# Optimization experiments

Hardware: AMD Instinct MI355X
Metric: run time of the kernel (lower is better)

Reference implementation:

```python
import jax, jax.numpy as jnp
import numpy as np

B, D, H, W = 16, 96, 96, 96
NUM_POINTS = 4096
THRESH = 0.5
CH = [3, 64, 128, 256, 512]   # shared-MLP channel progression (3 mlp layers + global_dim)
GROUPS = 8
EPS = 1e-5
HEAD_HIDDEN = 128


def setup_inputs() -> dict:
    key = jax.random.key(0)
    ks = jax.random.split(key, 8)
    inp = {"volume": jax.random.uniform(ks[0], (B, 1, D, H, W), jnp.float32)}
    for i in range(4):
        # Conv1d(kernel=1, no bias) weight (out, in); kaiming normal fan_out -> std=sqrt(2/out)
        inp[f"w{i+1}"] = jax.random.normal(ks[1 + i], (CH[i + 1], CH[i]), jnp.float32) * np.sqrt(2.0 / CH[i + 1]).astype(np.float32)
        inp[f"gn{i+1}_w"] = jnp.ones((CH[i + 1],), jnp.float32)
        inp[f"gn{i+1}_b"] = jnp.zeros((CH[i + 1],), jnp.float32)
    inp["fc1_w"] = jax.random.normal(ks[5], (HEAD_HIDDEN, CH[-1]), jnp.float32) * np.sqrt(2.0 / HEAD_HIDDEN).astype(np.float32)
    inp["fc1_b"] = jnp.zeros((HEAD_HIDDEN,), jnp.float32)
    inp["fc2_w"] = jax.random.normal(ks[6], (1, HEAD_HIDDEN), jnp.float32) * np.sqrt(2.0).astype(np.float32)
    inp["fc2_b"] = jnp.zeros((1,), jnp.float32)
    return inp


def volume_to_points(volume):
    """Batched, jit-safe version of volume_to_pointcloud (eval mode: linspace sampling)."""
    b, _, d, h, w = volume.shape
    mask = (volume[:, 0] > THRESH).reshape(b, -1)              # (B, D*H*W)
    n = mask.sum(axis=1)                                        # (B,) foreground counts
    # Stable argsort on ~mask puts foreground flat-indices first, in ascending order
    # == torch nonzero() ordering (row-major over D,H,W).
    order = jnp.argsort(jnp.logical_not(mask), axis=1, stable=True)  # (B, D*H*W)
    p = jnp.arange(NUM_POINTS)
    n_f = n.astype(jnp.float32)[:, None]
    # torch.linspace(0, n-1, P).long(): truncation toward zero
    lin = (p[None, :].astype(jnp.float32) * (n_f - 1.0) / (NUM_POINTS - 1)).astype(jnp.int32)
    lin = jnp.clip(lin, 0, jnp.maximum(n[:, None] - 1, 0))
    wrap = p[None, :] % jnp.maximum(n[:, None], 1)              # n < P fallback
    idx = jnp.where(n[:, None] >= NUM_POINTS, lin, wrap)        # (B, P)
    flat = jnp.take_along_axis(order, idx, axis=1)              # (B, P) flat voxel indices
    dd = flat // (h * w)
    hh = (flat // w) % h
    ww = flat % w
    coords = jnp.stack([dd, hh, ww], axis=1).astype(jnp.float32)  # (B, 3, P)
    scale = jnp.array([max(d - 1, 1), max(h - 1, 1), max(w - 1, 1)], jnp.float32)
    pts = coords / scale[None, :, None] * 2.0 - 1.0
    return jnp.where((n > 0)[:, None, None], pts, 0.0)


def group_norm(x, gamma, beta):
    b, c, npts = x.shape
    xg = x.reshape(b, GROUPS, c // GROUPS, npts)
    mu = xg.mean(axis=(2, 3), keepdims=True)
    var = xg.var(axis=(2, 3), keepdims=True)
    xn = ((xg - mu) * jax.lax.rsqrt(var + EPS)).reshape(b, c, npts)
    return xn * gamma[None, :, None] + beta[None, :, None]


def reference(volume, w1, gn1_w, gn1_b, w2, gn2_w, gn2_b, w3, gn3_w, gn3_b,
              w4, gn4_w, gn4_b, fc1_w, fc1_b, fc2_w, fc2_b):
    x = volume_to_points(volume)                                 # (B, 3, P)
    for cw, gw, gb in ((w1, gn1_w, gn1_b), (w2, gn2_w, gn2_b),
                       (w3, gn3_w, gn3_b), (w4, gn4_w, gn4_b)):
        x = jax.nn.relu(group_norm(jnp.einsum('oc,bcn->bon', cw, x), gw, gb))
    g = x.max(axis=2)                                            # (B, 512) global max-pool
    hdn = jax.nn.relu(g @ fc1_w.T + fc1_b)                       # dropout is identity in eval
    logits = (hdn @ fc2_w.T + fc2_b)[:, 0]                       # squeeze(-1) -> (B,)
    return logits
```

## Files before the change

### kernel.cpp

```cpp
#include <hip/hip_runtime.h>
#include <hip/hip_bf16.h>

#define NB 16
#define VOX 884736
#define NPTS 4096
#define CHUNK 1024
#define NCHUNK 864

typedef _Float16 f16x8 __attribute__((ext_vector_type(8)));
typedef _Float16 f16x4 __attribute__((ext_vector_type(4)));
typedef float f32x4 __attribute__((ext_vector_type(4)));

typedef const __attribute__((address_space(1))) _Float16 gf16;
typedef __attribute__((address_space(3))) _Float16 lf16;
#define GLOAD_LDS(gp, lp) __builtin_amdgcn_global_load_lds((gf16*)(gp), (lf16*)(lp), 16, 0, 0)

__device__ __forceinline__ f16x8 nrelu(f16x8 y, f16x8 sc, f16x8 sh) {
    f16x8 r = y * sc + sh;
    #pragma unroll
    for (int e = 0; e < 8; e++) r[e] = (r[e] > (_Float16)0.f) ? r[e] : (_Float16)0.f;
    return r;
}


__device__ inline void cast_chunk(const float* __restrict__ wf, _Float16* __restrict__ wh,
                                  int CIN, int t) {
    int lane = t & 63;
    int NCB = CIN / 32;
    int cb = (t >> 6) % NCB;
    int ob = t / (64 * NCB);
    int o = ob * 16 + (lane & 15);
    int c0 = cb * 32 + (lane >> 4) * 8;
    const float* src = wf + (size_t)o * CIN + c0;
    f16x8 v;
    #pragma unroll
    for (int e = 0; e < 8; e++) v[e] = (_Float16)src[e];
    *(f16x8*)(wh + (size_t)t * 8) = v;
}


__global__ __launch_bounds__(256) void count_cast_kernel(const float* __restrict__ vol,
                                                         int* __restrict__ counts,
                                                         unsigned long long* __restrict__ bits,
                                                         const float* __restrict__ w2,
                                                         const float* __restrict__ w3,
                                                         const float* __restrict__ w4,
                                                         _Float16* __restrict__ w2f,
                                                         _Float16* __restrict__ w3f,
                                                         _Float16* __restrict__ w4f) {
    if (blockIdx.x >= NB * NCHUNK) {
        int t = (blockIdx.x - NB * NCHUNK) * 256 + threadIdx.x;
        if (t < 1024) cast_chunk(w2, w2f, 64, t);
        else if (t < 1024 + 4096) cast_chunk(w3, w3f, 128, t - 1024);
        else if (t < 1024 + 4096 + 16384) cast_chunk(w4, w4f, 256, t - 5120);
        return;
    }
    int blk = blockIdx.x;
    const float4* v4 = (const float4*)(vol + (size_t)blk * CHUNK);
    float4 v = v4[threadIdx.x];
    int nib = (v.x > 0.5f) | ((v.y > 0.5f) << 1) | ((v.z > 0.5f) << 2) | ((v.w > 0.5f) << 3);
    __shared__ unsigned char nibs[256];
    nibs[threadIdx.x] = (unsigned char)nib;
    int cnt = __popc(nib);
    for (int off = 32; off; off >>= 1) cnt += __shfl_down(cnt, off, 64);
    __shared__ int s[4];
    if ((threadIdx.x & 63) == 0) s[threadIdx.x >> 6] = cnt;
    __syncthreads();
    if (threadIdx.x < 16) {
        unsigned long long wd = 0;
        #pragma unroll
        for (int i = 0; i < 16; i++)
            wd |= (unsigned long long)nibs[threadIdx.x * 16 + i] << (4 * i);
        bits[(size_t)blk * 16 + threadIdx.x] = wd;
    }
    if (threadIdx.x == 0) counts[blk] = s[0] + s[1] + s[2] + s[3];
}


__global__ __launch_bounds__(256) void points_kernel(const unsigned long long* __restrict__ bits,
                                                     const int* __restrict__ counts,
                                                     const float* __restrict__ w1,
                                                     float* __restrict__ pts,
                                                     float* __restrict__ pstat1) {
    int b = blockIdx.x >> 4;
    int pc = blockIdx.x & 15;
    int p = pc * 256 + threadIdx.x;
    int tid = threadIdx.x;
    __shared__ int sdat[NCHUNK];
    __shared__ float sw1[192];
    __shared__ int wsum[4];
    for (int i = tid; i < NCHUNK; i += 256) sdat[i] = counts[b * NCHUNK + i];
    if (tid < 192) sw1[tid] = w1[tid];
    __syncthreads();
    int i0 = tid * 4;
    int v0 = (i0 + 0 < NCHUNK) ? sdat[i0 + 0] : 0;
    int v1 = (i0 + 1 < NCHUNK) ? sdat[i0 + 1] : 0;
    int v2 = (i0 + 2 < NCHUNK) ? sdat[i0 + 2] : 0;
    int v3 = (i0 + 3 < NCHUNK) ? sdat[i0 + 3] : 0;
    int l3 = v0 + v1 + v2 + v3;
    int lane = tid & 63, wv = tid >> 6;
    int a = l3;
    #pragma unroll
    for (int off = 1; off < 64; off <<= 1) {
        int x = __shfl_up(a, off, 64);
        if (lane >= off) a += x;
    }
    if (lane == 63) wsum[wv] = a;
    __syncthreads();
    int woff = 0;
    #pragma unroll
    for (int w = 0; w < 4; w++) if (w < wv) woff += wsum[w];
    a += woff;
    int excl = a - l3;
    int n = wsum[0] + wsum[1] + wsum[2] + wsum[3];
    __syncthreads();
    if (i0 + 0 < NCHUNK) sdat[i0 + 0] = excl;
    if (i0 + 1 < NCHUNK) sdat[i0 + 1] = excl + v0;
    if (i0 + 2 < NCHUNK) sdat[i0 + 2] = excl + v0 + v1;
    if (i0 + 3 < NCHUNK) sdat[i0 + 3] = excl + v0 + v1 + v2;
    __syncthreads();
    float px = 0.f, py = 0.f, pz = 0.f;
    if (n > 0) {
        int k;
        if (n >= NPTS) {
            float t = (float)p * ((float)n - 1.0f);
            t = t / 4095.0f;
            k = (int)t;
            if (k > n - 1) k = n - 1;
            if (k < 0) k = 0;
        } else {
            k = p % n;
        }
        int lo = 0, hi = NCHUNK - 1;
        while (lo < hi) {
            int mid = (lo + hi + 1) >> 1;
            if (sdat[mid] <= k) lo = mid; else hi = mid - 1;
        }
        int rr = k - sdat[lo];
        const unsigned long long* wb = bits + ((size_t)b * NCHUNK + lo) * 16;
        unsigned long long chosen = 0;
        int wordidx = 0;
        bool found = false;
        #pragma unroll
        for (int w = 0; w < 16; w++) {
            unsigned long long m = wb[w];
            int pcnt = __popcll(m);
            bool take = (!found) && (rr < pcnt);
            if (take) { chosen = m; wordidx = w; found = true; }
            if (!found) rr -= pcnt;
        }
        int pos = 0;
        unsigned long long m64 = chosen;
        int c = __popcll(m64 & 0xFFFFFFFFull);
        if (rr >= c) { pos = 32; rr -= c; m64 >>= 32; }
        unsigned mm = (unsigned)m64;
        c = __popc(mm & 0xFFFFu); if (rr >= c) { pos += 16; rr -= c; mm >>= 16; }
        c = __popc(mm & 0xFFu);   if (rr >= c) { pos += 8;  rr -= c; mm >>= 8; }
        c = __popc(mm & 0xFu);    if (rr >= c) { pos += 4;  rr -= c; mm >>= 4; }
        c = __popc(mm & 0x3u);    if (rr >= c) { pos += 2;  rr -= c; mm >>= 2; }
        c = mm & 1u;              if (rr >= c) { pos += 1; }
        int flat = lo * CHUNK + wordidx * 64 + pos;
        int dd = flat / 9216;
        int rem = flat - dd * 9216;
        int hh = rem / 96;
        int ww = rem - hh * 96;
        px = (float)dd / 95.0f * 2.0f - 1.0f;
        py = (float)hh / 95.0f * 2.0f - 1.0f;
        pz = (float)ww / 95.0f * 2.0f - 1.0f;
    }
    pts[((size_t)b * 3 + 0) * NPTS + p] = px;
    pts[((size_t)b * 3 + 1) * NPTS + p] = py;
    pts[((size_t)b * 3 + 2) * NPTS + p] = pz;
    float s[8] = {}, q[8] = {};
    #pragma unroll
    for (int o = 0; o < 64; o++) {
        float av = sw1[o * 3 + 0] * px + sw1[o * 3 + 1] * py + sw1[o * 3 + 2] * pz;
        s[o >> 3] += av;
        q[o >> 3] += av * av;
    }
    __shared__ float red[4][8][2];
    #pragma unroll
    for (int g = 0; g < 8; g++) {
        float S = s[g], Q = q[g];
        for (int off = 32; off; off >>= 1) {
            S += __shfl_down(S, off, 64);
            Q += __shfl_down(Q, off, 64);
        }
        if ((threadIdx.x & 63) == 0) { red[wv][g][0] = S; red[wv][g][1] = Q; }
    }
    __syncthreads();
    if (tid < 8) {
        int g = tid;
        float S = red[0][g][0] + red[1][g][0] + red[2][g][0] + red[3][g][0];
        float Q = red[0][g][1] + red[1][g][1] + red[2][g][1] + red[3][g][1];
        float* d = pstat1 + (((size_t)(b * 8 + g)) * 16 + pc) * 2;
        d[0] = S; d[1] = Q;
    }
}


__global__ __launch_bounds__(256, 4) void fused_l2(const float* __restrict__ pts,
                                                   const float* __restrict__ w1,
                                                   const float* __restrict__ pstat1,
                                                   const float* __restrict__ gn1w,
                                                   const float* __restrict__ gn1b,
                                                   const _Float16* __restrict__ wfrag,
                                                   _Float16* __restrict__ y2,
                                                   float* __restrict__ pstat) {
    __shared__ _Float16 sl[64 * 64];
    __shared__ float sw1[192], ssc[64], ssh[64], ms1[8][2];
    int b = blockIdx.y, pblk = blockIdx.x, tid = threadIdx.x;
    if (tid < 192) sw1[tid] = w1[tid];
    if (tid < 8) {
        const float* pbase = pstat1 + (size_t)(b * 8 + tid) * 32;
        float S = 0.f, Q = 0.f;
        #pragma unroll
        for (int pc = 0; pc < 16; pc++) { S += pbase[2 * pc]; Q += pbase[2 * pc + 1]; }
        float inv = 1.0f / (8.0f * 4096.0f);
        float mu = S * inv;
        float var = Q * inv - mu * mu;
        if (var < 0.f) var = 0.f;
        ms1[tid][0] = mu; ms1[tid][1] = rsqrtf(var + 1e-5f);
    }
    __syncthreads();
    if (tid < 64) {
        int g = tid >> 3;
        float ga = gn1w[tid] * ms1[g][1];
        ssc[tid] = ga;
        ssh[tid] = gn1b[tid] - ms1[g][0] * ga;
    }
    __syncthreads();
    {
        int p = tid >> 2, qo = (tid & 3) * 16;
        int pg = pblk * 64 + p;
        float x0 = pts[((size_t)b * 3 + 0) * NPTS + pg];
        float x1 = pts[((size_t)b * 3 + 1) * NPTS + pg];
        float x2 = pts[((size_t)b * 3 + 2) * NPTS + pg];
        #pragma unroll
        for (int e = 0; e < 16; e++) {
            int o = qo + e;
            float a = sw1[o * 3 + 0] * x0 + sw1[o * 3 + 1] * x1 + sw1[o * 3 + 2] * x2;
            float r = fmaxf(a * ssc[o] + ssh[o], 0.f);
            sl[p * 64 + (((o >> 3) ^ (p & 7)) << 3) + (o & 7)] = (_Float16)r;
        }
    }
    __syncthreads();
    int wv = tid >> 6, lane = tid & 63, lr = lane & 15, lk = lane >> 4;
    int ph = wv & 1, oh = wv >> 1;
    int Pg = b * 64 + pblk;
    int pb32 = (Pg << 1) | ph;
    int P16 = Pg * 4 + ph * 2;
    f32x4 acc[2][4] = {};
    #pragma unroll
    for (int cb = 0; cb < 2; cb++) {
        int ch = cb * 4 + lk;
        f16x8 af0, af1;
        {
            int p0 = ph * 32 + lr;
            af0 = *(const f16x8*)(sl + p0 * 64 + ((ch ^ (p0 & 7)) << 3));
            int p1 = p0 + 16;
            af1 = *(const f16x8*)(sl + p1 * 64 + ((ch ^ (p1 & 7)) << 3));
        }
        #pragma unroll
        for (int i = 0; i < 4; i++) {
            int ofr = oh * 4 + i;
            f16x8 bf = *(const f16x8*)(wfrag + (((size_t)ofr * 2 + cb) * 64 + lane) * 8);
            acc[0][i] = __builtin_amdgcn_mfma_f32_16x16x32_f16(bf, af0, acc[0][i], 0, 0, 0);
            acc[1][i] = __builtin_amdgcn_mfma_f32_16x16x32_f16(bf, af1, acc[1][i], 0, 0, 0);
        }
    }
    #pragma unroll
    for (int i = 0; i < 4; i++) {
        int ofr = oh * 4 + i;
        int cb2 = ofr >> 1;
        int kg = (ofr & 1) * 2 + (lk >> 1);
        int lanep = lr + 16 * kg;
        int sub = lk & 1;
        #pragma unroll
        for (int pf = 0; pf < 2; pf++) {
            f16x4 vv;
            #pragma unroll
            for (int j = 0; j < 4; j++) vv[j] = (_Float16)acc[pf][i][j];
            *(f16x4*)(y2 + (((size_t)(P16 + pf) * 4 + cb2) * 64 + lanep) * 8 + sub * 4) = vv;
        }
        float s[4], q[4];
        #pragma unroll
        for (int j = 0; j < 4; j++) {
            float a0 = acc[0][i][j], a1 = acc[1][i][j];
            s[j] = a0 + a1; q[j] = a0 * a0 + a1 * a1;
        }
        #pragma unroll
        for (int m = 1; m <= 8; m <<= 1)
            #pragma unroll
            for (int j = 0; j < 4; j++) {
                s[j] += __shfl_xor(s[j], m, 64);
                q[j] += __shfl_xor(q[j], m, 64);
            }
        if (lr == 0) {
            int o0 = ofr * 16 + lk * 4;
            float* d = pstat + ((size_t)pb32 * 128 + o0) * 2;
            *(float4*)d = make_float4(s[0], q[0], s[1], q[1]);
            *(float4*)(d + 4) = make_float4(s[2], q[2], s[3], q[3]);
        }
    }
}


__global__ __launch_bounds__(256, 4) void fused_l3(const _Float16* __restrict__ y2,
                                                   const float* __restrict__ pstatIn,
                                                   const float* __restrict__ gn2w,
                                                   const float* __restrict__ gn2b,
                                                   const _Float16* __restrict__ w3f,
                                                   _Float16* __restrict__ y3,
                                                   float* __restrict__ pstatOut) {
    __shared__ _Float16 sl[64 * 128];
    __shared__ float sstat[256];
    __shared__ float ms[8][2];
    __shared__ _Float16 sscf[128], sshf[128];
    int b = blockIdx.y, pblk = blockIdx.x, tid = threadIdx.x;
    int wv = tid >> 6, lane = tid & 63, lr = lane & 15, lk = lane >> 4;
    int Pg = b * 64 + pblk;
    const _Float16* yt = y2 + (size_t)Pg * 64 * 128;
    #pragma unroll
    for (int i = 0; i < 4; i++) {
        int off = (wv * 4 + i) * 512;
        GLOAD_LDS(yt + off + lane * 8, sl + off);
    }
    {
        const float* slab = pstatIn + (size_t)b * 128 * 256;
        float acc = 0.f;
        #pragma unroll 8
        for (int pb = 0; pb < 128; pb++) acc += slab[pb * 256 + tid];
        sstat[tid] = acc;
    }
    __syncthreads();
    if (tid < 8) {
        float S = 0.f, Q = 0.f;
        #pragma unroll
        for (int i = 0; i < 16; i++) {
            int c = tid * 16 + i;
            S += sstat[2 * c]; Q += sstat[2 * c + 1];
        }
        float inv = 1.0f / (16.0f * 4096.0f);
        float mu = S * inv;
        float var = Q * inv - mu * mu;
        if (var < 0.f) var = 0.f;
        ms[tid][0] = mu; ms[tid][1] = rsqrtf(var + 1e-5f);
    }
    __syncthreads();
    if (tid < 128) {
        int g = tid >> 4;
        float ga = gn2w[tid] * ms[g][1];
        sscf[tid] = (_Float16)ga;
        sshf[tid] = (_Float16)(gn2b[tid] - ms[g][0] * ga);
    }
    __syncthreads();
    f16x8 scv[4], shv[4];
    #pragma unroll
    for (int cb = 0; cb < 4; cb++) {
        scv[cb] = *(const f16x8*)(sscf + cb * 32 + lk * 8);
        shv[cb] = *(const f16x8*)(sshf + cb * 32 + lk * 8);
    }
    int ph = wv & 1, oh = wv >> 1;
    int pb32 = (Pg << 1) | ph;
    int P16 = Pg * 4 + ph * 2;
    #pragma unroll
    for (int ck = 0; ck < 2; ck++) {
        f32x4 acc[2][4] = {};
        #pragma unroll
        for (int cb = 0; cb < 4; cb++) {
            f16x8 af0 = nrelu(*(const f16x8*)(sl + (((ph * 2 + 0) * 4 + cb) * 64 + lane) * 8), scv[cb], shv[cb]);
            f16x8 af1 = nrelu(*(const f16x8*)(sl + (((ph * 2 + 1) * 4 + cb) * 64 + lane) * 8), scv[cb], shv[cb]);
            #pragma unroll
            for (int i = 0; i < 4; i++) {
                int ofr = oh * 8 + ck * 4 + i;
                f16x8 bf = *(const f16x8*)(w3f + (((size_t)ofr * 4 + cb) * 64 + lane) * 8);
                acc[0][i] = __builtin_amdgcn_mfma_f32_16x16x32_f16(bf, af0, acc[0][i], 0, 0, 0);
                acc[1][i] = __builtin_amdgcn_mfma_f32_16x16x32_f16(bf, af1, acc[1][i], 0, 0, 0);
            }
        }
        #pragma unroll
        for (int i = 0; i < 4; i++) {
            int ofr = oh * 8 + ck * 4 + i;
            int cb3 = ofr >> 1;
            int kg = (ofr & 1) * 2 + (lk >> 1);
            int lanep = lr + 16 * kg;
            int sub = lk & 1;
            #pragma unroll
            for (int pf = 0; pf < 2; pf++) {
                f16x4 vv;
                #pragma unroll
                for (int j = 0; j < 4; j++) vv[j] = (_Float16)acc[pf][i][j];
                *(f16x4*)(y3 + (((size_t)(P16 + pf) * 8 + cb3) * 64 + lanep) * 8 + sub * 4) = vv;
            }
            float s[4], q[4];
            #pragma unroll
            for (int j = 0; j < 4; j++) {
                float a0 = acc[0][i][j], a1 = acc[1][i][j];
                s[j] = a0 + a1; q[j] = a0 * a0 + a1 * a1;
            }
            #pragma unroll
            for (int m = 1; m <= 8; m <<= 1)
                #pragma unroll
                for (int j = 0; j < 4; j++) {
                    s[j] += __shfl_xor(s[j], m, 64);
                    q[j] += __shfl_xor(q[j], m, 64);
                }
            if (lr == 0) {
                int o0 = ofr * 16 + lk * 4;
                float* d = pstatOut + ((size_t)pb32 * 256 + o0) * 2;
                *(float4*)d = make_float4(s[0], q[0], s[1], q[1]);
                *(float4*)(d + 4) = make_float4(s[2], q[2], s[3], q[3]);
            }
        }
    }
}


__global__ __launch_bounds__(256, 4) void fused_l4(const _Float16* __restrict__ y3,
                                                   const float* __restrict__ pstatIn,
                                                   const float* __restrict__ gn3w,
                                                   const float* __restrict__ gn3b,
                                                   const _Float16* __restrict__ w4f,
                                                   float* __restrict__ pstat4) {
    __shared__ _Float16 sl[64 * 256];
    __shared__ float sstat[512];
    __shared__ float ms[8][2];
    __shared__ _Float16 sscf[256], sshf[256];
    int b = blockIdx.y, pblk = blockIdx.x, tid = threadIdx.x;
    int wv = tid >> 6, lane = tid & 63, lr = lane & 15, lk = lane >> 4;
    int Pg = b * 64 + pblk;
    const _Float16* yt = y3 + (size_t)Pg * 64 * 256;
    #pragma unroll
    for (int i = 0; i < 8; i++) {
        int off = (wv * 8 + i) * 512;
        GLOAD_LDS(yt + off + lane * 8, sl + off);
    }
    {
        const float* slab = pstatIn + (size_t)b * 128 * 512;
        float a0 = 0.f, a1 = 0.f;
        #pragma unroll 8
        for (int pb = 0; pb < 128; pb++) {
            a0 += slab[pb * 512 + tid];
            a1 += slab[pb * 512 + tid + 256];
        }
        sstat[tid] = a0;
        sstat[tid + 256] = a1;
    }
    __syncthreads();
    if (tid < 8) {
        float S = 0.f, Q = 0.f;
        #pragma unroll
        for (int i = 0; i < 32; i++) {
            int c = tid * 32 + i;
            S += sstat[2 * c]; Q += sstat[2 * c + 1];
        }
        float inv = 1.0f / (32.0f * 4096.0f);
        float mu = S * inv;
        float var = Q * inv - mu * mu;
        if (var < 0.f) var = 0.f;
        ms[tid][0] = mu; ms[tid][1] = rsqrtf(var + 1e-5f);
    }
    __syncthreads();
    {
        int g = tid >> 5;
        float ga = gn3w[tid] * ms[g][1];
        sscf[tid] = (_Float16)ga;
        sshf[tid] = (_Float16)(gn3b[tid] - ms[g][0] * ga);
    }
    __syncthreads();
    int ph = wv & 1, oh = wv >> 1;
    int pb32 = (Pg << 1) | ph;
    #pragma unroll
    for (int ck = 0; ck < 4; ck++) {
        f32x4 acc[2][4] = {};
        #pragma unroll
        for (int cb = 0; cb < 8; cb++) {
            f16x8 scv = *(const f16x8*)(sscf + cb * 32 + lk * 8);
            f16x8 shv = *(const f16x8*)(sshf + cb * 32 + lk * 8);
            f16x8 af0 = nrelu(*(const f16x8*)(sl + (((ph * 2 + 0) * 8 + cb) * 64 + lane) * 8), scv, shv);
            f16x8 af1 = nrelu(*(const f16x8*)(sl + (((ph * 2 + 1) * 8 + cb) * 64 + lane) * 8), scv, shv);
            #pragma unroll
            for (int i = 0; i < 4; i++) {
                int ofr = oh * 16 + ck * 4 + i;
                f16x8 bf = *(const f16x8*)(w4f + (((size_t)ofr * 8 + cb) * 64 + lane) * 8);
                acc[0][i] = __builtin_amdgcn_mfma_f32_16x16x32_f16(af0, bf, acc[0][i], 0, 0, 0);
                acc[1][i] = __builtin_amdgcn_mfma_f32_16x16x32_f16(af1, bf, acc[1][i], 0, 0, 0);
            }
        }
        #pragma unroll
        for (int i = 0; i < 4; i++) {
            int ofr = oh * 16 + ck * 4 + i;
            float S = 0.f, Q = 0.f, MX = -1e30f, MN = 1e30f;
            #pragma unroll
            for (int pf = 0; pf < 2; pf++)
                #pragma unroll
                for (int j = 0; j < 4; j++) {
                    float v = acc[pf][i][j];
                    S += v; Q += v * v;
                    MX = fmaxf(MX, v); MN = fminf(MN, v);
                }
            S += __shfl_xor(S, 16, 64); Q += __shfl_xor(Q, 16, 64);
            MX = fmaxf(MX, __shfl_xor(MX, 16, 64)); MN = fminf(MN, __shfl_xor(MN, 16, 64));
            S += __shfl_xor(S, 32, 64); Q += __shfl_xor(Q, 32, 64);
            MX = fmaxf(MX, __shfl_xor(MX, 32, 64)); MN = fminf(MN, __shfl_xor(MN, 32, 64));
            if (lk == 0) {
                int o = ofr * 16 + lr;
                *(float4*)(pstat4 + ((size_t)pb32 * 512 + o) * 4) = make_float4(S, Q, MX, MN);
            }
        }
    }
}


__global__ __launch_bounds__(256) void pool_final(const float* __restrict__ pstat4,
                                                  const float* __restrict__ gamma,
                                                  const float* __restrict__ beta,
                                                  float* __restrict__ g) {
    int b = blockIdx.x >> 3, gr = blockIdx.x & 7;
    int ch = threadIdx.x & 63;
    int pg = threadIdx.x >> 6;
    int o = gr * 64 + ch;
    float S = 0.f, Q = 0.f, MX = -1e30f, MN = 1e30f;
    for (int pb = pg; pb < 128; pb += 4) {
        float4 v = *(const float4*)(pstat4 + (((size_t)(b * 128 + pb)) * 512 + o) * 4);
        S += v.x; Q += v.y; MX = fmaxf(MX, v.z); MN = fminf(MN, v.w);
    }
    __shared__ float sS[4][64], sQ[4][64], sMX[4][64], sMN[4][64];
    sS[pg][ch] = S; sQ[pg][ch] = Q; sMX[pg][ch] = MX; sMN[pg][ch] = MN;
    __syncthreads();
    if (threadIdx.x < 64) {
        float Sc = sS[0][ch] + sS[1][ch] + sS[2][ch] + sS[3][ch];
        float Qc = sQ[0][ch] + sQ[1][ch] + sQ[2][ch] + sQ[3][ch];
        float MXc = fmaxf(fmaxf(sMX[0][ch], sMX[1][ch]), fmaxf(sMX[2][ch], sMX[3][ch]));
        float MNc = fminf(fminf(sMN[0][ch], sMN[1][ch]), fminf(sMN[2][ch], sMN[3][ch]));
        float St = Sc, Qt = Qc;
        for (int off = 32; off; off >>= 1) {
            St += __shfl_xor(St, off, 64);
            Qt += __shfl_xor(Qt, off, 64);
        }
        float inv = 1.0f / (64.0f * 4096.0f);
        float mu = St * inv;
        float var = Qt * inv - mu * mu;
        if (var < 0.f) var = 0.f;
        float rstd = rsqrtf(var + 1e-5f);
        float sc = gamma[o] * rstd;
        float sh = beta[o] - mu * sc;
        float m = (sc >= 0.f ? MXc : MNc) * sc + sh;
        g[b * 512 + o] = fmaxf(m, 0.f);
    }
}


__global__ __launch_bounds__(128) void head_kernel(const float* __restrict__ g,
                                                   const float* __restrict__ fc1w,
                                                   const float* __restrict__ fc1b,
                                                   const float* __restrict__ fc2w,
                                                   const float* __restrict__ fc2b,
                                                   float* __restrict__ out) {
    int b = blockIdx.x;
    int o = threadIdx.x;
    __shared__ float sg[512];
    for (int i = threadIdx.x; i < 512; i += 128) sg[i] = g[b * 512 + i];
    __syncthreads();
    float acc = fc1b[o];
    for (int c = 0; c < 512; c++) acc += sg[c] * fc1w[o * 512 + c];
    float h = fmaxf(acc, 0.f) * fc2w[o];
    for (int off = 32; off; off >>= 1) h += __shfl_down(h, off, 64);
    __shared__ float s2[2];
    if ((threadIdx.x & 63) == 0) s2[threadIdx.x >> 6] = h;
    __syncthreads();
    if (threadIdx.x == 0) out[b] = s2[0] + s2[1] + fc2b[0];
}


extern "C" void kernel_launch(void* const* d_in, const int* in_sizes, int n_in,
                              void* d_out, int out_size, void* d_ws, size_t ws_size,
                              hipStream_t stream) {
    const float* vol  = (const float*)d_in[0];
    const float* w1   = (const float*)d_in[1];
    const float* gn1w = (const float*)d_in[2];
    const float* gn1b = (const float*)d_in[3];
    const float* w2   = (const float*)d_in[4];
    const float* gn2w = (const float*)d_in[5];
    const float* gn2b = (const float*)d_in[6];
    const float* w3   = (const float*)d_in[7];
    const float* gn3w = (const float*)d_in[8];
    const float* gn3b = (const float*)d_in[9];
    const float* w4   = (const float*)d_in[10];
    const float* gn4w = (const float*)d_in[11];
    const float* gn4b = (const float*)d_in[12];
    const float* fc1w = (const float*)d_in[13];
    const float* fc1b = (const float*)d_in[14];
    const float* fc2w = (const float*)d_in[15];
    const float* fc2b = (const float*)d_in[16];
    float* out = (float*)d_out;

    char* ws = (char*)d_ws;
    size_t cur = 0;
    auto alloc = [&](size_t bytes) -> void* {
        cur = (cur + 255) & ~(size_t)255;
        void* p = ws + cur;
        cur += bytes;
        return p;
    };
    int*      counts  = (int*)alloc((size_t)NB * NCHUNK * 4);
    unsigned long long* bits = (unsigned long long*)alloc((size_t)NB * NCHUNK * 16 * 8);
    float*    pts     = (float*)alloc((size_t)NB * 3 * NPTS * 4);
    float*    gbuf    = (float*)alloc((size_t)NB * 512 * 4);
    float*    pstat1  = (float*)alloc((size_t)NB * 8 * 16 * 2 * 4);
    float*    pstatG  = (float*)alloc((size_t)NB * 128 * 128 * 2 * 4);
    float*    pstatG2 = (float*)alloc((size_t)NB * 128 * 256 * 2 * 4);
    float*    pstat4  = (float*)alloc((size_t)NB * 128 * 512 * 4 * 4);
    _Float16* w2f     = (_Float16*)alloc((size_t)128 * 64 * 2);
    _Float16* w3f     = (_Float16*)alloc((size_t)256 * 128 * 2);
    _Float16* w4f     = (_Float16*)alloc((size_t)512 * 256 * 2);
    _Float16* y2      = (_Float16*)alloc((size_t)NB * NPTS * 128 * 2);
    _Float16* y3      = (_Float16*)alloc((size_t)NB * NPTS * 256 * 2);

    count_cast_kernel<<<dim3(NB * NCHUNK + 84), dim3(256), 0, stream>>>(
        vol, counts, bits, w2, w3, w4, w2f, w3f, w4f);

    points_kernel<<<dim3(NB * 16), dim3(256), 0, stream>>>(bits, counts, w1, pts, pstat1);

    fused_l2<<<dim3(64, NB), dim3(256), 0, stream>>>(pts, w1, pstat1, gn1w, gn1b, w2f, y2, pstatG);

    fused_l3<<<dim3(64, NB), dim3(256), 0, stream>>>(y2, pstatG, gn2w, gn2b, w3f, y3, pstatG2);

    fused_l4<<<dim3(64, NB), dim3(256), 0, stream>>>(y3, pstatG2, gn3w, gn3b, w4f, pstat4);

    pool_final<<<dim3(NB * 8), dim3(256), 0, stream>>>(pstat4, gn4w, gn4b, gbuf);
    head_kernel<<<dim3(NB), dim3(128), 0, stream>>>(gbuf, fc1w, fc1b, fc2w, fc2b, out);
}
```

Measured before the change: 125.5 us.

## Hoist GroupNorm stat reduction into separate finalize kernels; pre-normalize tiles in LDS

Before, every block of fused_l3 and fused_l4 re-reduced the full per-batch partial-stat slab, which is redundant across the 64 blocks of each batch. That reduction now runs once per (batch, group) in a new gn_finalizeG kernel, which writes fp16 scale and shift vectors. The consumer kernels then apply the norm and ReLU once to the LDS tile in place, instead of inside the MFMA inner loop where it was repeated for each output chunk. This adds two kernel launches and an extra LDS read-write pass plus barrier in exchange.

Measured after the change: 119.5 us, median of 2. 4.8% less time.

```diff
diff --git a/kernel.cpp b/kernel.cpp
--- a/kernel.cpp
+++ b/kernel.cpp
@@ -306,16 +306,59 @@
 }
 
 
+template <int C>
+__global__ __launch_bounds__(256) void gn_finalizeG(const float* __restrict__ pstat,
+                                                    const float* __restrict__ gamma,
+                                                    const float* __restrict__ beta,
+                                                    _Float16* __restrict__ scaleh,
+                                                    _Float16* __restrict__ shifth) {
+    constexpr int GS = C / 8;
+    int b = blockIdx.x >> 3, g = blockIdx.x & 7;
+    const float* base = pstat + (size_t)b * 128 * C * 2;
+    float S = 0.f, Q = 0.f;
+    for (int i = threadIdx.x; i < 128 * GS; i += 256) {
+        int pb = i / GS;
+        int c = g * GS + (i % GS);
+        const float* d = base + ((size_t)pb * C + c) * 2;
+        S += d[0]; Q += d[1];
+    }
+    for (int off = 32; off; off >>= 1) {
+        S += __shfl_down(S, off, 64);
+        Q += __shfl_down(Q, off, 64);
+    }
+    __shared__ float ss[8];
+    if ((threadIdx.x & 63) == 0) {
+        ss[(threadIdx.x >> 6) * 2] = S;
+        ss[(threadIdx.x >> 6) * 2 + 1] = Q;
+    }
+    __syncthreads();
+    __shared__ float ms[2];
+    if (threadIdx.x == 0) {
+        float St = ss[0] + ss[2] + ss[4] + ss[6];
+        float Qt = ss[1] + ss[3] + ss[5] + ss[7];
+        float inv = 1.0f / ((float)GS * 4096.0f);
+        float mu = St * inv;
+        float var = Qt * inv - mu * mu;
+        if (var < 0.f) var = 0.f;
+        ms[0] = mu; ms[1] = rsqrtf(var + 1e-5f);
+    }
+    __syncthreads();
+    for (int i = threadIdx.x; i < GS; i += 256) {
+        int c = g * GS + i;
+        float ga = gamma[c] * ms[1];
+        scaleh[(size_t)b * C + c] = (_Float16)ga;
+        shifth[(size_t)b * C + c] = (_Float16)(beta[c] - ms[0] * ga);
+    }
+}
+
+
 __global__ __launch_bounds__(256, 4) void fused_l3(const _Float16* __restrict__ y2,
-                                                   const float* __restrict__ pstatIn,
-                                                   const float* __restrict__ gn2w,
-                                                   const float* __restrict__ gn2b,
+                                                   const _Float16* __restrict__ sch,
+                                                   const _Float16* __restrict__ shh,
                                                    const _Float16* __restrict__ w3f,
                                                    _Float16* __restrict__ y3,
                                                    float* __restrict__ pstatOut) {
     __shared__ _Float16 sl[64 * 128];
-    __shared__ float sstat[256];
-    __shared__ float ms[8][2];
     __shared__ _Float16 sscf[128], sshf[128];
     int b = blockIdx.y, pblk = blockIdx.x, tid = threadIdx.x;
     int wv = tid >> 6, lane = tid & 63, lr = lane & 15, lk = lane >> 4;
@@ -326,41 +369,23 @@
         int off = (wv * 4 + i) * 512;
         GLOAD_LDS(yt + off + lane * 8, sl + off);
     }
-    {
-        const float* slab = pstatIn + (size_t)b * 128 * 256;
-        float acc = 0.f;
-        #pragma unroll 8
-        for (int pb = 0; pb < 128; pb++) acc += slab[pb * 256 + tid];
-        sstat[tid] = acc;
-    }
-    __syncthreads();
-    if (tid < 8) {
-        float S = 0.f, Q = 0.f;
-        #pragma unroll
-        for (int i = 0; i < 16; i++) {
-            int c = tid * 16 + i;
-            S += sstat[2 * c]; Q += sstat[2 * c + 1];
-        }
-        float inv = 1.0f / (16.0f * 4096.0f);
-        float mu = S * inv;
-        float var = Q * inv - mu * mu;
-        if (var < 0.f) var = 0.f;
-        ms[tid][0] = mu; ms[tid][1] = rsqrtf(var + 1e-5f);
-    }
-    __syncthreads();
     if (tid < 128) {
-        int g = tid >> 4;
-        float ga = gn2w[tid] * ms[g][1];
-        sscf[tid] = (_Float16)ga;
-        sshf[tid] = (_Float16)(gn2b[tid] - ms[g][0] * ga);
-    }
-    __syncthreads();
-    f16x8 scv[4], shv[4];
-    #pragma unroll
-    for (int cb = 0; cb < 4; cb++) {
-        scv[cb] = *(const f16x8*)(sscf + cb * 32 + lk * 8);
-        shv[cb] = *(const f16x8*)(sshf + cb * 32 + lk * 8);
-    }
+        sscf[tid] = sch[b * 128 + tid];
+        sshf[tid] = shh[b * 128 + tid];
+    }
+    __syncthreads();
+    #pragma unroll
+    for (int k = 0; k < 4; k++) {
+        int q = tid + k * 256;
+        int ln = q & 63;
+        int cb = (q >> 6) & 3;
+        int c0 = cb * 32 + (ln >> 4) * 8;
+        f16x8 v = *(const f16x8*)(sl + (size_t)q * 8);
+        f16x8 scv = *(const f16x8*)(sscf + c0);
+        f16x8 shv = *(const f16x8*)(sshf + c0);
+        *(f16x8*)(sl + (size_t)q * 8) = nrelu(v, scv, shv);
+    }
+    __syncthreads();
     int ph = wv & 1, oh = wv >> 1;
     int pb32 = (Pg << 1) | ph;
     int P16 = Pg * 4 + ph * 2;
@@ -369,8 +394,8 @@
         f32x4 acc[2][4] = {};
         #pragma unroll
         for (int cb = 0; cb < 4; cb++) {
-            f16x8 af0 = nrelu(*(const f16x8*)(sl + (((ph * 2 + 0) * 4 + cb) * 64 + lane) * 8), scv[cb], shv[cb]);
-            f16x8 af1 = nrelu(*(const f16x8*)(sl + (((ph * 2 + 1) * 4 + cb) * 64 + lane) * 8), scv[cb], shv[cb]);
+            f16x8 af0 = *(const f16x8*)(sl + (((ph * 2 + 0) * 4 + cb) * 64 + lane) * 8);
+            f16x8 af1 = *(const f16x8*)(sl + (((ph * 2 + 1) * 4 + cb) * 64 + lane) * 8);
             #pragma unroll
             for (int i = 0; i < 4; i++) {
                 int ofr = oh * 8 + ck * 4 + i;
@@ -418,14 +443,11 @@
 
 
 __global__ __launch_bounds__(256, 4) void fused_l4(const _Float16* __restrict__ y3,
-                                                   const float* __restrict__ pstatIn,
-                                                   const float* __restrict__ gn3w,
-                                                   const float* __restrict__ gn3b,
+                                                   const _Float16* __restrict__ sch,
+                                                   const _Float16* __restrict__ shh,
                                                    const _Float16* __restrict__ w4f,
                                                    float* __restrict__ pstat4) {
     __shared__ _Float16 sl[64 * 256];
-    __shared__ float sstat[512];
-    __shared__ float ms[8][2];
     __shared__ _Float16 sscf[256], sshf[256];
     int b = blockIdx.y, pblk = blockIdx.x, tid = threadIdx.x;
     int wv = tid >> 6, lane = tid & 63, lr = lane & 15, lk = lane >> 4;
@@ -436,37 +458,19 @@
         int off = (wv * 8 + i) * 512;
         GLOAD_LDS(yt + off + lane * 8, sl + off);
     }
-    {
-        const float* slab = pstatIn + (size_t)b * 128 * 512;
-        float a0 = 0.f, a1 = 0.f;
-        #pragma unroll 8
-        for (int pb = 0; pb < 128; pb++) {
-            a0 += slab[pb * 512 + tid];
-            a1 += slab[pb * 512 + tid + 256];
-        }
-        sstat[tid] = a0;
-        sstat[tid + 256] = a1;
-    }
-    __syncthreads();
-    if (tid < 8) {
-        float S = 0.f, Q = 0.f;
-        #pragma unroll
-        for (int i = 0; i < 32; i++) {
-            int c = tid * 32 + i;
-            S += sstat[2 * c]; Q += sstat[2 * c + 1];
-        }
-        float inv = 1.0f / (32.0f * 4096.0f);
-        float mu = S * inv;
-        float var = Q * inv - mu * mu;
-        if (var < 0.f) var = 0.f;
-        ms[tid][0] = mu; ms[tid][1] = rsqrtf(var + 1e-5f);
-    }
-    __syncthreads();
-    {
-        int g = tid >> 5;
-        float ga = gn3w[tid] * ms[g][1];
-        sscf[tid] = (_Float16)ga;
-        sshf[tid] = (_Float16)(gn3b[tid] - ms[g][0] * ga);
+    sscf[tid] = sch[b * 256 + tid];
+    sshf[tid] = shh[b * 256 + tid];
+    __syncthreads();
+    #pragma unroll
+    for (int k = 0; k < 8; k++) {
+        int q = tid + k * 256;
+        int ln = q & 63;
+        int cb = (q >> 6) & 7;
+        int c0 = cb * 32 + (ln >> 4) * 8;
+        f16x8 v = *(const f16x8*)(sl + (size_t)q * 8);
+        f16x8 scv = *(const f16x8*)(sscf + c0);
+        f16x8 shv = *(const f16x8*)(sshf + c0);
+        *(f16x8*)(sl + (size_t)q * 8) = nrelu(v, scv, shv);
     }
     __syncthreads();
     int ph = wv & 1, oh = wv >> 1;
@@ -476,10 +480,8 @@
         f32x4 acc[2][4] = {};
         #pragma unroll
         for (int cb = 0; cb < 8; cb++) {
-            f16x8 scv = *(const f16x8*)(sscf + cb * 32 + lk * 8);
-            f16x8 shv = *(const f16x8*)(sshf + cb * 32 + lk * 8);
-            f16x8 af0 = nrelu(*(const f16x8*)(sl + (((ph * 2 + 0) * 8 + cb) * 64 + lane) * 8), scv, shv);
-            f16x8 af1 = nrelu(*(const f16x8*)(sl + (((ph * 2 + 1) * 8 + cb) * 64 + lane) * 8), scv, shv);
+            f16x8 af0 = *(const f16x8*)(sl + (((ph * 2 + 0) * 8 + cb) * 64 + lane) * 8);
+            f16x8 af1 = *(const f16x8*)(sl + (((ph * 2 + 1) * 8 + cb) * 64 + lane) * 8);
             #pragma unroll
             for (int i = 0; i < 4; i++) {
                 int ofr = oh * 16 + ck * 4 + i;
@@ -612,6 +614,10 @@
     float*    pstatG  = (float*)alloc((size_t)NB * 128 * 128 * 2 * 4);
     float*    pstatG2 = (float*)alloc((size_t)NB * 128 * 256 * 2 * 4);
     float*    pstat4  = (float*)alloc((size_t)NB * 128 * 512 * 4 * 4);
+    _Float16* sc2h    = (_Float16*)alloc((size_t)NB * 128 * 2);
+    _Float16* sh2h    = (_Float16*)alloc((size_t)NB * 128 * 2);
+    _Float16* sc3h    = (_Float16*)alloc((size_t)NB * 256 * 2);
+    _Float16* sh3h    = (_Float16*)alloc((size_t)NB * 256 * 2);
     _Float16* w2f     = (_Float16*)alloc((size_t)128 * 64 * 2);
     _Float16* w3f     = (_Float16*)alloc((size_t)256 * 128 * 2);
     _Float16* w4f     = (_Float16*)alloc((size_t)512 * 256 * 2);
@@ -625,9 +631,11 @@
 
     fused_l2<<<dim3(64, NB), dim3(256), 0, stream>>>(pts, w1, pstat1, gn1w, gn1b, w2f, y2, pstatG);
 
-    fused_l3<<<dim3(64, NB), dim3(256), 0, stream>>>(y2, pstatG, gn2w, gn2b, w3f, y3, pstatG2);
-
-    fused_l4<<<dim3(64, NB), dim3(256), 0, stream>>>(y3, pstatG2, gn3w, gn3b, w4f, pstat4);
+    gn_finalizeG<128><<<dim3(NB * 8), dim3(256), 0, stream>>>(pstatG, gn2w, gn2b, sc2h, sh2h);
+    fused_l3<<<dim3(64, NB), dim3(256), 0, stream>>>(y2, sc2h, sh2h, w3f, y3, pstatG2);
+
+    gn_finalizeG<256><<<dim3(NB * 8), dim3(256), 0, stream>>>(pstatG2, gn3w, gn3b, sc3h, sh3h);
+    fused_l4<<<dim3(64, NB), dim3(256), 0, stream>>>(y3, sc3h, sh3h, w4f, pstat4);
 
     pool_final<<<dim3(NB * 8), dim3(256), 0, stream>>>(pstat4, gn4w, gn4b, gbuf);
     head_kernel<<<dim3(NB), dim3(128), 0, stream>>>(gbuf, fc1w, fc1b, fc2w, fc2b, out);
```
